# Kernel optimization log

Measured on AMD Instinct MI355X. Metric: run time of the kernel, lower is better.

Reference implementation:

```python
import jax, jax.numpy as jnp
import numpy as np

B, IN_DIM, HID, SUB_IN, SUB_OUT, GRID = 4096, 256, 512, 256, 256, 32
LN_EPS = 1e-5


def setup_inputs() -> dict:
    key = jax.random.key(0)
    ks = jax.random.split(key, 16)
    inp = {
        'x':  jax.random.normal(ks[0], (B, IN_DIM), jnp.float32),
        'h0': jax.random.normal(ks[1], (B, HID), jnp.float32),
        'c0': jax.random.normal(ks[2], (B, HID), jnp.float32),
        's0': jax.random.normal(ks[3], (B, SUB_OUT), jnp.float32),
        # LSTM gate params
        'kernel':  jax.random.normal(ks[4], (IN_DIM, 3 * HID), jnp.float32) * 0.05,
        'rkernel': jax.random.normal(ks[5], (HID, 3 * HID), jnp.float32) * 0.05,
        'bias':    jnp.zeros((3 * HID,), jnp.float32),
        # sub-layer recurrent mixing kernels (num_sub_layers=1)
        'sub_kx': jax.random.normal(ks[6], (1, IN_DIM, SUB_IN), jnp.float32) * 0.05,
        'sub_kh': jax.random.normal(ks[7], (1, SUB_OUT, SUB_IN), jnp.float32) * 0.05,
        'sub_tkan_kernel': jax.random.normal(ks[8], (1, 2 * SUB_OUT), jnp.float32) * 0.05,
        # Fourier KAN coefficients: (2, outdim, indim, gridsize) + bias
        'fc': jax.random.normal(ks[9], (2, SUB_OUT, SUB_IN, GRID), jnp.float32) / np.sqrt(SUB_IN * GRID),
        'fb': jnp.zeros((SUB_OUT,), jnp.float32),
        # aggregation + layer norm
        'agg_w': jax.random.normal(ks[10], (SUB_OUT, HID), jnp.float32) * 0.05,
        'agg_b': jnp.zeros((HID,), jnp.float32),
        'ln_g':  jnp.ones((HID,), jnp.float32),
        'ln_b':  jnp.zeros((HID,), jnp.float32),
    }
    return inp


def _fourier_kan(z, fc, fb):
    # z: [B, SUB_IN] -> [B, SUB_OUT]
    k = jnp.arange(1, GRID + 1, dtype=z.dtype)          # [G]
    ang = z[:, :, None] * k                             # [B, IN, G]
    return (jnp.einsum('big,oig->bo', jnp.cos(ang), fc[0])
            + jnp.einsum('big,oig->bo', jnp.sin(ang), fc[1]) + fb)


def reference(x, h0, c0, s0, kernel, rkernel, bias, sub_kx, sub_kh,
              sub_tkan_kernel, fc, fb, agg_w, agg_b, ln_g, ln_b):
    # LSTM-style gates (note: candidate also passes through sigmoid then tanh,
    # exactly as in the torch source)
    gates = jax.nn.sigmoid(x @ kernel + h0 @ rkernel + bias)      # [B, 3H]
    i, f, c_cand = jnp.split(gates, 3, axis=-1)
    c = f * c0 + i * jnp.tanh(c_cand)                             # [B, H]

    # single KAN sub-layer
    agg_in = x @ sub_kx[0] + s0 @ sub_kh[0]                       # [B, SUB_IN]
    sub_out = _fourier_kan(agg_in, fc, fb)                        # [B, SUB_OUT]
    rk_h, rk_x = jnp.split(sub_tkan_kernel[0], 2)                 # [SUB_OUT] each
    new_s = rk_h * sub_out + s0 * rk_x

    # aggregation -> output gate
    o = jax.nn.sigmoid(sub_out @ agg_w + agg_b)                   # [B, H]
    h = o * jnp.tanh(c)

    # layer norm
    mu = jnp.mean(h, axis=-1, keepdims=True)
    var = jnp.mean(jnp.square(h - mu), axis=-1, keepdims=True)
    h = (h - mu) * jax.lax.rsqrt(var + LN_EPS) * ln_g + ln_b
    return (h, c, new_s)
```

## Files before the change

### kernel.cpp

```cpp
#include <hip/hip_runtime.h>
#include <hip/hip_bf16.h>

typedef __bf16 bf16_t;
typedef __bf16 bf16x2 __attribute__((ext_vector_type(2)));
typedef __bf16 bf16x4 __attribute__((ext_vector_type(4)));
typedef __bf16 bf16x8 __attribute__((ext_vector_type(8)));
typedef float  f32x4  __attribute__((ext_vector_type(4)));

#define NB 4096
#define IN_DIM 256
#define HID 512
#define SUB 256
#define GRID_ 32

__device__ __forceinline__ float fract_f(float x) {
#if __has_builtin(__builtin_amdgcn_fractf)
  return __builtin_amdgcn_fractf(x);
#else
  return x - floorf(x);
#endif
}
__device__ __forceinline__ float cos_rev(float rev) {
#if __has_builtin(__builtin_amdgcn_cosf)
  return __builtin_amdgcn_cosf(rev);
#else
  return __cosf(rev * 6.283185307179586f);
#endif
}
__device__ __forceinline__ float sin_rev(float rev) {
#if __has_builtin(__builtin_amdgcn_sinf)
  return __builtin_amdgcn_sinf(rev);
#else
  return __sinf(rev * 6.283185307179586f);
#endif
}
__device__ __forceinline__ float sigm(float v) { return 1.f / (1.f + __expf(-v)); }
__device__ __forceinline__ float fast_tanh(float x) {
  float e = __expf(2.f * x);
  return (e - 1.f) / (e + 1.f);
}
#define INV2PI 0.15915494309189535f

#define O_XHI   0ull
#define O_XLO   2097152ull
#define O_H0    4194304ull
#define O_S0H   8388608ull
#define O_S0L   10485760ull
#define O_FCB   12582912ull
#define O_O     12582912ull
#define O_KT    20971520ull
#define O_RKT   21757952ull
#define O_AWT   23330816ull
#define O_KXH   23592960ull
#define O_KXL   23724032ull
#define O_KHH   23855104ull
#define O_KHL   23986176ull
#define O_TC    24117248ull
#define O_SOB   32505856ull
#define O_AGG   34603008ull
#define O_P3    38797312ull

__device__ __forceinline__ void tconv_body(const float* __restrict__ src,
                                           bf16_t* __restrict__ hi,
                                           bf16_t* __restrict__ lo,
                                           int R, int C, int bx, int by,
                                           bool wantlo, float scale) {
  __shared__ float t[32][33];
  int c0 = bx * 32, r0 = by * 32;
  int tx = threadIdx.x & 31, ty = threadIdx.x >> 5;
#pragma unroll
  for (int rr = 0; rr < 4; rr++) {
    int r = ty + rr * 8;
    t[r][tx] = src[(size_t)(r0 + r) * C + c0 + tx];
  }
  __syncthreads();
#pragma unroll
  for (int rr = 0; rr < 4; rr++) {
    int cl = ty + rr * 8;
    float f = t[tx][cl] * scale;
    bf16_t h = (bf16_t)f;
    size_t oi = (size_t)(c0 + cl) * R + r0 + tx;
    hi[oi] = h;
    if (wantlo) lo[oi] = (bf16_t)(f - (float)h);
  }
}

__global__ __launch_bounds__(256) void k_prep(const float* __restrict__ x,
                                              const float* __restrict__ h0,
                                              const float* __restrict__ s0,
                                              const float* __restrict__ fc,
                                              const float* __restrict__ Wk,
                                              const float* __restrict__ Wr,
                                              const float* __restrict__ aw,
                                              const float* __restrict__ kx,
                                              const float* __restrict__ kh,
                                              bf16_t* __restrict__ xhi, bf16_t* __restrict__ xlo,
                                              bf16_t* __restrict__ h0b,
                                              bf16_t* __restrict__ s0h, bf16_t* __restrict__ s0l,
                                              bf16_t* __restrict__ fcb2,
                                              bf16_t* __restrict__ kt,
                                              bf16_t* __restrict__ rkt,
                                              bf16_t* __restrict__ awt,
                                              bf16_t* __restrict__ kxh, bf16_t* __restrict__ kxl,
                                              bf16_t* __restrict__ khh, bf16_t* __restrict__ khl) {
  int bid = blockIdx.x;
  if (bid < 1024) {
    for (int q = bid * 256 + threadIdx.x; q < 1048576; q += 262144) {
      const float* src; bf16_t* hi; bf16_t* lo = nullptr; int base;
      if (q < 262144)       { src = x;  hi = xhi; lo = xlo; base = q; }
      else if (q < 786432)  { src = h0; hi = h0b;           base = q - 262144; }
      else                  { src = s0; hi = s0h; lo = s0l; base = q - 786432; }
      float4 v = *(const float4*)(src + (size_t)base * 4);
      bf16x4 h; h[0] = (bf16_t)v.x; h[1] = (bf16_t)v.y; h[2] = (bf16_t)v.z; h[3] = (bf16_t)v.w;
      *(bf16x4*)(hi + (size_t)base * 4) = h;
      if (lo) {
        bf16x4 l;
        l[0] = (bf16_t)(v.x - (float)h[0]); l[1] = (bf16_t)(v.y - (float)h[1]);
        l[2] = (bf16_t)(v.z - (float)h[2]); l[3] = (bf16_t)(v.w - (float)h[3]);
        *(bf16x4*)(lo + (size_t)base * 4) = l;
      }
    }
  } else if (bid < 3072) {
    __shared__ float tf[64 * 36];
    int tt = bid - 1024;
    int s = tt & 1, ot = (tt >> 1) & 3, i = tt >> 3;
    int o0 = ot * 64, nbb = ot >> 1, wnn = ot & 1;
    int row = threadIdx.x >> 2, col = (threadIdx.x & 3) * 8;
    const float* src = fc + ((size_t)s << 21) + ((size_t)(o0 + row) << 13) +
                       ((size_t)i << 5) + col;
    float4 v0 = *(const float4*)(src);
    float4 v1 = *(const float4*)(src + 4);
    *(float4*)(tf + row * 36 + col) = v0;
    *(float4*)(tf + row * 36 + col + 4) = v1;
    __syncthreads();
    int lr = threadIdx.x & 15, g4 = (threadIdx.x >> 4) & 3, j = threadIdx.x >> 6;
    const float* rp = tf + (j * 16 + lr) * 36 + g4 * 8;
    float4 a = *(const float4*)(rp);
    float4 b = *(const float4*)(rp + 4);
    bf16x8 h;
    h[0] = (bf16_t)a.x; h[1] = (bf16_t)a.y; h[2] = (bf16_t)a.z; h[3] = (bf16_t)a.w;
    h[4] = (bf16_t)b.x; h[5] = (bf16_t)b.y; h[6] = (bf16_t)b.z; h[7] = (bf16_t)b.w;
    size_t idx = (size_t)i * 16384 + nbb * 8192 + wnn * 4096 + j * 1024 +
                 s * 512 + g4 * 128 + lr * 8;
    *(bf16x8*)(fcb2 + idx) = h;
  } else {
    int b = bid - 3072;
    if (b < 384)       { tconv_body(Wk, kt,  nullptr, 256, 1536, b % 48, b / 48, false, 1.f); }
    else if (b < 1152) { b -= 384;  tconv_body(Wr, rkt, nullptr, 512, 1536, b % 48, b / 48, false, 1.f); }
    else if (b < 1280) { b -= 1152; tconv_body(aw, awt, nullptr, 256, 512,  b % 16, b / 16, false, 1.f); }
    else if (b < 1344) { b -= 1280; tconv_body(kx, kxh, kxl,     256, 256,  b % 8,  b / 8,  true, INV2PI); }
    else               { b -= 1344; tconv_body(kh, khh, khl,     256, 256,  b % 8,  b / 8,  true, INV2PI); }
  }
}

struct Pass { const bf16_t* A; const bf16_t* Bt; int K; int lda; int ldbt; };
struct GArgs {
  Pass p[6]; int np;
  const float* bias;
  int act;
  float* out; bf16_t* outb; int ldout;
};

template<int BM, int BN>
__global__ __launch_bounds__(512) void k_gemm(GArgs g) {
  constexpr int MI = BM / 32;
  constexpr int NJ = BN / 64;
  constexpr int IA = (BM * 8) / 512;
  constexpr int IB = (BN * 8) / 512;
  __shared__ bf16_t smA[BM * 64];
  __shared__ bf16_t smB[BN * 64];
  const int tid = threadIdx.x;
  const int m0 = blockIdx.y * BM, n0 = blockIdx.x * BN;
  const int wv = tid >> 6, lane = tid & 63;
  const int wm = wv >> 2, wn = wv & 3;
  const int lr = lane & 15, g4 = lane >> 4;

  f32x4 acc[MI][NJ];
#pragma unroll
  for (int i = 0; i < MI; i++)
#pragma unroll
    for (int j = 0; j < NJ; j++) acc[i][j] = f32x4{0.f, 0.f, 0.f, 0.f};

  for (int ps = 0; ps < g.np; ps++) {
    const bf16_t* A = g.p[ps].A;
    const bf16_t* Bt = g.p[ps].Bt;
    const int K = g.p[ps].K, lda = g.p[ps].lda, ldbt = g.p[ps].ldbt;
    for (int k0 = 0; k0 < K; k0 += 64) {
      bf16x8 ar[IA], br[IB];
#pragma unroll
      for (int r = 0; r < IA; r++) {
        int task = tid + r * 512, row = task >> 3, t = task & 7, sf = t ^ (row & 7);
        ar[r] = *(const bf16x8*)(A + (size_t)(m0 + row) * lda + k0 + sf * 8);
      }
#pragma unroll
      for (int r = 0; r < IB; r++) {
        int task = tid + r * 512, row = task >> 3, t = task & 7, sf = t ^ (row & 7);
        br[r] = *(const bf16x8*)(Bt + (size_t)(n0 + row) * ldbt + k0 + sf * 8);
      }
      __syncthreads();
#pragma unroll
      for (int r = 0; r < IA; r++) {
        int task = tid + r * 512, row = task >> 3, t = task & 7;
        *(bf16x8*)(smA + row * 64 + t * 8) = ar[r];
      }
#pragma unroll
      for (int r = 0; r < IB; r++) {
        int task = tid + r * 512, row = task >> 3, t = task & 7;
        *(bf16x8*)(smB + row * 64 + t * 8) = br[r];
      }
      __syncthreads();
#pragma unroll
      for (int ks = 0; ks < 2; ks++) {
        bf16x8 af[MI], bfr[NJ];
#pragma unroll
        for (int i = 0; i < MI; i++) {
          int row = wm * (BM / 2) + i * 16 + lr;
          af[i] = *(const bf16x8*)(smA + row * 64 + ((ks * 4 + g4) ^ (lr & 7)) * 8);
        }
#pragma unroll
        for (int j = 0; j < NJ; j++) {
          int row = wn * (BN / 4) + j * 16 + lr;
          bfr[j] = *(const bf16x8*)(smB + row * 64 + ((ks * 4 + g4) ^ (lr & 7)) * 8);
        }
#pragma unroll
        for (int i = 0; i < MI; i++)
#pragma unroll
          for (int j = 0; j < NJ; j++)
            acc[i][j] = __builtin_amdgcn_mfma_f32_16x16x32_bf16(af[i], bfr[j], acc[i][j], 0, 0, 0);
      }
    }
  }
#pragma unroll
  for (int i = 0; i < MI; i++)
#pragma unroll
    for (int j = 0; j < NJ; j++) {
      int col = n0 + wn * (BN / 4) + j * 16 + lr;
      float bb = g.bias ? g.bias[col] : 0.f;
#pragma unroll
      for (int r = 0; r < 4; r++) {
        int row = m0 + wm * (BM / 2) + i * 16 + (lane >> 4) * 4 + r;
        float v = acc[i][j][r] + bb;
        if (g.act == 1) v = sigm(v);
        if (g.outb) g.outb[(size_t)row * g.ldout + col] = (bf16_t)v;
        else        g.out [(size_t)row * g.ldout + col] = v;
      }
    }
}

struct GAArgs {
  const bf16_t* xhi; const bf16_t* h0b; const bf16_t* kt; const bf16_t* rkt;
  const float* bias; const float* c0; float* c_out; bf16_t* tc;
  const bf16_t* aggA[6]; const bf16_t* aggB[6];
  float* agg;
};

__global__ __launch_bounds__(256, 2) void k_gatesagg(GAArgs ga) {
  __shared__ bf16_t smA[64 * 64];
  __shared__ bf16_t smB[3 * 64 * 64];
  const int tid = threadIdx.x;
  const int wv = tid >> 6, lane = tid & 63;
  const int wm = wv >> 1, wn = wv & 1;
  const int lr = lane & 15, g4 = lane >> 4;

  if (blockIdx.x < 512) {
    const int b = blockIdx.x;
    const int n0 = (b & 7) * 64, m0 = (b >> 3) * 64;
    f32x4 acc[3][2][2];
#pragma unroll
    for (int t = 0; t < 3; t++)
#pragma unroll
      for (int i = 0; i < 2; i++)
#pragma unroll
        for (int j = 0; j < 2; j++) acc[t][i][j] = f32x4{0.f, 0.f, 0.f, 0.f};

    for (int ps = 0; ps < 2; ps++) {
      const bf16_t* A  = ps ? ga.h0b : ga.xhi;
      const bf16_t* Bt = ps ? ga.rkt : ga.kt;
      const int K = ps ? 512 : 256, ld = K;
      for (int k0 = 0; k0 < K; k0 += 64) {
        bf16x8 ar[2], br[6];
#pragma unroll
        for (int r = 0; r < 2; r++) {
          int task = tid + r * 256, row = task >> 3, t = task & 7, sf = t ^ (row & 7);
          ar[r] = *(const bf16x8*)(A + (size_t)(m0 + row) * ld + k0 + sf * 8);
        }
#pragma unroll
        for (int r = 0; r < 6; r++) {
          int task = tid + r * 256;
          int gate = task >> 9, rem = task & 511, o = rem >> 3, t = rem & 7, sf = t ^ (o & 7);
          br[r] = *(const bf16x8*)(Bt + (size_t)(gate * 512 + n0 + o) * ld + k0 + sf * 8);
        }
        __syncthreads();
#pragma unroll
        for (int r = 0; r < 2; r++) {
          int task = tid + r * 256, row = task >> 3, t = task & 7;
          *(bf16x8*)(smA + row * 64 + t * 8) = ar[r];
        }
#pragma unroll
        for (int r = 0; r < 6; r++) {
          int task = tid + r * 256;
          int gate = task >> 9, rem = task & 511, o = rem >> 3, t = rem & 7;
          *(bf16x8*)(smB + (gate * 64 + o) * 64 + t * 8) = br[r];
        }
        __syncthreads();
#pragma unroll
        for (int ks = 0; ks < 2; ks++) {
          bf16x8 af[2];
#pragma unroll
          for (int i = 0; i < 2; i++) {
            int row = wm * 32 + i * 16 + lr;
            af[i] = *(const bf16x8*)(smA + row * 64 + ((ks * 4 + g4) ^ (lr & 7)) * 8);
          }
#pragma unroll
          for (int t = 0; t < 3; t++) {
            bf16x8 bfr[2];
#pragma unroll
            for (int j = 0; j < 2; j++) {
              int row = wn * 32 + j * 16 + lr;
              bfr[j] = *(const bf16x8*)(smB + (t * 64 + row) * 64 + ((ks * 4 + g4) ^ (lr & 7)) * 8);
            }
#pragma unroll
            for (int i = 0; i < 2; i++)
#pragma unroll
              for (int j = 0; j < 2; j++)
                acc[t][i][j] = __builtin_amdgcn_mfma_f32_16x16x32_bf16(af[i], bfr[j], acc[t][i][j], 0, 0, 0);
          }
        }
      }
    }
#pragma unroll
    for (int i = 0; i < 2; i++)
#pragma unroll
      for (int j = 0; j < 2; j++) {
        int col = n0 + wn * 32 + j * 16 + lr;
        float bi = ga.bias[col], bf_ = ga.bias[512 + col], bc = ga.bias[1024 + col];
#pragma unroll
        for (int r = 0; r < 4; r++) {
          int row = m0 + wm * 32 + i * 16 + g4 * 4 + r;
          size_t idx = (size_t)row * 512 + col;
          float iv = sigm(acc[0][i][j][r] + bi);
          float fv = sigm(acc[1][i][j][r] + bf_);
          float cc = sigm(acc[2][i][j][r] + bc);
          float cv = fv * ga.c0[idx] + iv * fast_tanh(cc);
          ga.c_out[idx] = cv;
          ga.tc[idx] = (bf16_t)fast_tanh(cv);
        }
      }
  } else {
    const int b = blockIdx.x - 512;
    const int n0 = (b & 3) * 64, m0 = (b >> 2) * 64;
    f32x4 acc[2][2];
#pragma unroll
    for (int i = 0; i < 2; i++)
#pragma unroll
      for (int j = 0; j < 2; j++) acc[i][j] = f32x4{0.f, 0.f, 0.f, 0.f};

    for (int ps = 0; ps < 6; ps++) {
      const bf16_t* A  = ga.aggA[ps];
      const bf16_t* Bt = ga.aggB[ps];
      for (int k0 = 0; k0 < 256; k0 += 64) {
        bf16x8 ar[2], br[2];
#pragma unroll
        for (int r = 0; r < 2; r++) {
          int task = tid + r * 256, row = task >> 3, t = task & 7, sf = t ^ (row & 7);
          ar[r] = *(const bf16x8*)(A  + (size_t)(m0 + row) * 256 + k0 + sf * 8);
          br[r] = *(const bf16x8*)(Bt + (size_t)(n0 + row) * 256 + k0 + sf * 8);
        }
        __syncthreads();
#pragma unroll
        for (int r = 0; r < 2; r++) {
          int task = tid + r * 256, row = task >> 3, t = task & 7;
          *(bf16x8*)(smA + row * 64 + t * 8) = ar[r];
          *(bf16x8*)(smB + row * 64 + t * 8) = br[r];
        }
        __syncthreads();
#pragma unroll
        for (int ks = 0; ks < 2; ks++) {
          bf16x8 af[2], bfr[2];
#pragma unroll
          for (int i = 0; i < 2; i++) {
            int row = wm * 32 + i * 16 + lr;
            af[i] = *(const bf16x8*)(smA + row * 64 + ((ks * 4 + g4) ^ (lr & 7)) * 8);
          }
#pragma unroll
          for (int j = 0; j < 2; j++) {
            int row = wn * 32 + j * 16 + lr;
            bfr[j] = *(const bf16x8*)(smB + row * 64 + ((ks * 4 + g4) ^ (lr & 7)) * 8);
          }
#pragma unroll
          for (int i = 0; i < 2; i++)
#pragma unroll
            for (int j = 0; j < 2; j++)
              acc[i][j] = __builtin_amdgcn_mfma_f32_16x16x32_bf16(af[i], bfr[j], acc[i][j], 0, 0, 0);
        }
      }
    }
#pragma unroll
    for (int i = 0; i < 2; i++)
#pragma unroll
      for (int j = 0; j < 2; j++) {
        int col = n0 + wn * 32 + j * 16 + lr;
#pragma unroll
        for (int r = 0; r < 4; r++) {
          int row = m0 + wm * 32 + i * 16 + g4 * 4 + r;
          ga.agg[(size_t)row * 256 + col] = acc[i][j][r];
        }
      }
  }
}

struct FArgs { const float* agg; const bf16_t* fcb2; bf16_t* P[8]; };

__global__ __launch_bounds__(128, 2) void k_fourier(FArgs fa) {
  __shared__ float  zl[64 * 33];
  __shared__ bf16_t Asm[2][64 * 64];
  const int tid = threadIdx.x;
  const int bx = blockIdx.x;
  const int q = bx & 7, nb = (bx >> 3) & 1, mb = bx >> 4;
  const int m0 = mb * 64, n0 = nb * 128, i0 = q * 32;
  const int wv = tid >> 6, lane = tid & 63;
  const int wn = wv;
  const int lr = lane & 15, g4 = lane >> 4;

#pragma unroll
  for (int r = 0; r < 4; r++) {
    int task = tid + r * 128, row = task >> 3, seg = task & 7;
    float4 v = *(const float4*)(fa.agg + (size_t)(m0 + row) * 256 + i0 + seg * 4);
    zl[row * 33 + seg * 4 + 0] = v.x;
    zl[row * 33 + seg * 4 + 1] = v.y;
    zl[row * 33 + seg * 4 + 2] = v.z;
    zl[row * 33 + seg * 4 + 3] = v.w;
  }

  const bf16_t* pB = fa.fcb2 + (size_t)i0 * 16384 + nb * 8192 + wn * 4096 + lane * 8;
  auto loadB = [&](int i, bf16x8 (&b)[8]) {
#pragma unroll
    for (int ks = 0; ks < 2; ks++)
#pragma unroll
      for (int j = 0; j < 4; j++)
        b[ks * 4 + j] = *(const bf16x8*)(pB + (size_t)i * 16384 + j * 1024 + ks * 512);
  };

  const int grow = tid >> 1, hp = tid & 1;
  const float* zp = zl + grow * 33;
  const int as0 = grow * 64 + (((2 * hp    ) ^ (grow & 7)) * 8);
  const int as1 = grow * 64 + (((2 * hp + 1) ^ (grow & 7)) * 8);
  const int as2 = grow * 64 + (((4 + 2 * hp) ^ (grow & 7)) * 8);
  const int as3 = grow * 64 + (((5 + 2 * hp) ^ (grow & 7)) * 8);
  auto genA = [&](int i, bf16_t* Ab) {
    float zr = zp[i];
    bf16x8 c0v, c1v, s0v, s1v;
#pragma unroll
    for (int t = 0; t < 8; t++) {
      float r0 = fract_f(zr * (float)(hp * 16 + t + 1));
      float r1 = fract_f(zr * (float)(hp * 16 + 8 + t + 1));
      c0v[t] = (bf16_t)cos_rev(r0); s0v[t] = (bf16_t)sin_rev(r0);
      c1v[t] = (bf16_t)cos_rev(r1); s1v[t] = (bf16_t)sin_rev(r1);
    }
    *(bf16x8*)(Ab + as0) = c0v;
    *(bf16x8*)(Ab + as1) = c1v;
    *(bf16x8*)(Ab + as2) = s0v;
    *(bf16x8*)(Ab + as3) = s1v;
  };

  int offA[8];
#pragma unroll
  for (int ks = 0; ks < 2; ks++)
#pragma unroll
    for (int i4 = 0; i4 < 4; i4++)
      offA[ks * 4 + i4] = (i4 * 16 + lr) * 64 + ((ks * 4 + g4) ^ (lr & 7)) * 8;

  f32x4 acc[4][4];
#pragma unroll
  for (int i = 0; i < 4; i++)
#pragma unroll
    for (int j = 0; j < 4; j++) acc[i][j] = f32x4{0.f, 0.f, 0.f, 0.f};

  auto domfma = [&](const bf16x8 (&af)[8], const bf16x8 (&b)[8]) {
    __builtin_amdgcn_s_setprio(1);
#pragma unroll
    for (int ks = 0; ks < 2; ks++)
#pragma unroll
      for (int i4 = 0; i4 < 4; i4++)
#pragma unroll
        for (int j = 0; j < 4; j++)
          acc[i4][j] = __builtin_amdgcn_mfma_f32_16x16x32_bf16(af[ks * 4 + i4], b[ks * 4 + j], acc[i4][j], 0, 0, 0);
    __builtin_amdgcn_s_setprio(0);
  };
  auto readA = [&](const bf16_t* Ac, bf16x8 (&af)[8]) {
#pragma unroll
    for (int t = 0; t < 8; t++) af[t] = *(const bf16x8*)(Ac + offA[t]);
  };

  bf16x8 bA_[8], bB_[8];
  __syncthreads();
  loadB(0, bA_);
  genA(0, Asm[0]);
  asm volatile("s_waitcnt lgkmcnt(0)" ::: "memory");
  __builtin_amdgcn_s_barrier();

#pragma unroll 1
  for (int it = 0; it < 16; it++) {
    const int i = it * 2;
    bf16x8 af[8];
    if (i < 31) loadB(i + 1, bB_);
    readA(Asm[0], af);
    if (i < 31) genA(i + 1, Asm[1]);
    domfma(af, bA_);
    asm volatile("s_waitcnt lgkmcnt(0)" ::: "memory");
    __builtin_amdgcn_s_barrier();
    if (i + 2 < 32) loadB(i + 2, bA_);
    readA(Asm[1], af);
    if (i + 2 < 32) genA(i + 2, Asm[0]);
    domfma(af, bB_);
    asm volatile("s_waitcnt lgkmcnt(0)" ::: "memory");
    __builtin_amdgcn_s_barrier();
  }

  bf16_t* outp = fa.P[q];
#pragma unroll
  for (int i = 0; i < 4; i++)
#pragma unroll
    for (int j = 0; j < 4; j++) {
      int col = n0 + wn * 64 + j * 16 + lr;
#pragma unroll
      for (int r = 0; r < 4; r++) {
        int row = m0 + i * 16 + g4 * 4 + r;
        outp[(size_t)row * 256 + col] = (bf16_t)acc[i][j][r];
      }
    }
}

struct RArgs {
  const bf16_t* P[8];
  const float* fb; const float* tk; const float* s0;
  float* news; bf16_t* sob;
};

__global__ __launch_bounds__(256) void k_freduce(RArgs ra) {
  int stride = gridDim.x * blockDim.x;
  for (int qd = blockIdx.x * blockDim.x + threadIdx.x; qd < 262144; qd += stride) {
    int i = qd * 4, o = i & 255;
    float4 v = {0.f, 0.f, 0.f, 0.f};
#pragma unroll
    for (int c = 0; c < 8; c++) {
      bf16x4 p = *(const bf16x4*)(ra.P[c] + i);
      v.x += (float)p[0]; v.y += (float)p[1]; v.z += (float)p[2]; v.w += (float)p[3];
    }
    v.x += ra.fb[o + 0]; v.y += ra.fb[o + 1]; v.z += ra.fb[o + 2]; v.w += ra.fb[o + 3];
    bf16x4 sb; sb[0] = (bf16_t)v.x; sb[1] = (bf16_t)v.y; sb[2] = (bf16_t)v.z; sb[3] = (bf16_t)v.w;
    *(bf16x4*)(ra.sob + i) = sb;
    float4 s = *(const float4*)(ra.s0 + i);
    float4 ns;
    ns.x = ra.tk[o + 0] * v.x + ra.tk[256 + o + 0] * s.x;
    ns.y = ra.tk[o + 1] * v.y + ra.tk[256 + o + 1] * s.y;
    ns.z = ra.tk[o + 2] * v.z + ra.tk[256 + o + 2] * s.z;
    ns.w = ra.tk[o + 3] * v.w + ra.tk[256 + o + 3] * s.w;
    *(float4*)(ra.news + i) = ns;
  }
}

__global__ __launch_bounds__(256) void k_ln(const bf16_t* __restrict__ o,
                                            const bf16_t* __restrict__ tc,
                                            const float* __restrict__ lg,
                                            const float* __restrict__ lb,
                                            float* __restrict__ h) {
  int b = blockIdx.x, tid = threadIdx.x;
  bf16x2 ov = *(const bf16x2*)(o + (size_t)b * 512 + tid * 2);
  bf16x2 tv = *(const bf16x2*)(tc + (size_t)b * 512 + tid * 2);
  float h0 = (float)ov[0] * (float)tv[0], h1 = (float)ov[1] * (float)tv[1];
  float s = h0 + h1, ss = h0 * h0 + h1 * h1;
#pragma unroll
  for (int off = 32; off; off >>= 1) {
    s += __shfl_xor(s, off);
    ss += __shfl_xor(ss, off);
  }
  __shared__ float red[8];
  int wid = tid >> 6;
  if ((tid & 63) == 0) { red[wid] = s; red[4 + wid] = ss; }
  __syncthreads();
  s = red[0] + red[1] + red[2] + red[3];
  ss = red[4] + red[5] + red[6] + red[7];
  float mu = s * (1.f / 512.f);
  float var = ss * (1.f / 512.f) - mu * mu;
  float rs = rsqrtf(var + 1e-5f);
  int j = tid * 2;
  h[(size_t)b * 512 + j]     = (h0 - mu) * rs * lg[j]     + lb[j];
  h[(size_t)b * 512 + j + 1] = (h1 - mu) * rs * lg[j + 1] + lb[j + 1];
}

extern "C" void kernel_launch(void* const* d_in, const int* in_sizes, int n_in,
                              void* d_out, int out_size, void* d_ws, size_t ws_size,
                              hipStream_t stream) {
  const float* x    = (const float*)d_in[0];
  const float* h0   = (const float*)d_in[1];
  const float* c0   = (const float*)d_in[2];
  const float* s0   = (const float*)d_in[3];
  const float* Wk   = (const float*)d_in[4];
  const float* Wr   = (const float*)d_in[5];
  const float* bias = (const float*)d_in[6];
  const float* kx   = (const float*)d_in[7];
  const float* kh   = (const float*)d_in[8];
  const float* tk   = (const float*)d_in[9];
  const float* fc   = (const float*)d_in[10];
  const float* fb   = (const float*)d_in[11];
  const float* aw   = (const float*)d_in[12];
  const float* ab   = (const float*)d_in[13];
  const float* lg   = (const float*)d_in[14];
  const float* lbp  = (const float*)d_in[15];
  float* out = (float*)d_out;
  char* ws = (char*)d_ws;
  auto BF = [&](unsigned long long off) { return (bf16_t*)(ws + off); };
  auto FP = [&](unsigned long long off) { return (float*)(ws + off); };

  k_prep<<<4480, 256, 0, stream>>>(x, h0, s0, fc, Wk, Wr, aw, kx, kh,
                                   BF(O_XHI), BF(O_XLO), BF(O_H0),
                                   BF(O_S0H), BF(O_S0L), BF(O_FCB),
                                   BF(O_KT), BF(O_RKT), BF(O_AWT),
                                   BF(O_KXH), BF(O_KXL), BF(O_KHH), BF(O_KHL));

  {
    GAArgs ga{};
    ga.xhi = BF(O_XHI); ga.h0b = BF(O_H0); ga.kt = BF(O_KT); ga.rkt = BF(O_RKT);
    ga.bias = bias; ga.c0 = c0; ga.c_out = out + 2097152; ga.tc = BF(O_TC);
    ga.aggA[0] = BF(O_XHI); ga.aggB[0] = BF(O_KXH);
    ga.aggA[1] = BF(O_XHI); ga.aggB[1] = BF(O_KXL);
    ga.aggA[2] = BF(O_XLO); ga.aggB[2] = BF(O_KXH);
    ga.aggA[3] = BF(O_S0H); ga.aggB[3] = BF(O_KHH);
    ga.aggA[4] = BF(O_S0H); ga.aggB[4] = BF(O_KHL);
    ga.aggA[5] = BF(O_S0L); ga.aggB[5] = BF(O_KHH);
    ga.agg = FP(O_AGG);
    k_gatesagg<<<768, 256, 0, stream>>>(ga);
  }

  FArgs fa;
  fa.agg = FP(O_AGG); fa.fcb2 = BF(O_FCB);
  for (int c = 0; c < 6; c++) fa.P[c] = BF((unsigned long long)c * 2097152ull);
  fa.P[6] = BF(O_P3);
  fa.P[7] = BF(O_P3 + 2097152ull);
  k_fourier<<<1024, 128, 0, stream>>>(fa);

  RArgs ra;
  for (int c = 0; c < 8; c++) ra.P[c] = fa.P[c];
  ra.fb = fb; ra.tk = tk; ra.s0 = s0;
  ra.news = out + 4194304; ra.sob = BF(O_SOB);
  k_freduce<<<1024, 256, 0, stream>>>(ra);

  {
    GArgs g{};
    g.p[0] = { BF(O_SOB), BF(O_AWT), 256, 256, 256 };
    g.np = 1; g.bias = ab; g.act = 1;
    g.out = nullptr; g.outb = BF(O_O); g.ldout = 512;
    k_gemm<64, 128><<<dim3(4, 64), 512, 0, stream>>>(g);
  }
  k_ln<<<4096, 256, 0, stream>>>(BF(O_O), BF(O_TC), lg, lbp, out);
}
```

Baseline: 95.88 us.

## Fuse Fourier partial reduction and new_s update into output-projection GEMM

Removes the separate reduction kernel. The sigmoid output-projection GEMM now sums the eight bf16 partial Fourier buffers while loading its A tile, adds the bias, and the first column-block also writes new_s. This eliminates one kernel launch and the intermediate bf16 sub_out buffer round-trip. In exchange, each of the four N-blocks re-reads all partial buffers, quadrupling the partial-sum reads, which must be served from cache to pay off.

```diff
diff --git a/kernel.cpp b/kernel.cpp
--- a/kernel.cpp
+++ b/kernel.cpp
@@ -56,7 +56,6 @@
 #define O_KHH   23855104ull
 #define O_KHL   23986176ull
 #define O_TC    24117248ull
-#define O_SOB   32505856ull
 #define O_AGG   34603008ull
 #define O_P3    38797312ull
 
@@ -153,100 +152,6 @@
   }
 }
 
-struct Pass { const bf16_t* A; const bf16_t* Bt; int K; int lda; int ldbt; };
-struct GArgs {
-  Pass p[6]; int np;
-  const float* bias;
-  int act;
-  float* out; bf16_t* outb; int ldout;
-};
-
-template<int BM, int BN>
-__global__ __launch_bounds__(512) void k_gemm(GArgs g) {
-  constexpr int MI = BM / 32;
-  constexpr int NJ = BN / 64;
-  constexpr int IA = (BM * 8) / 512;
-  constexpr int IB = (BN * 8) / 512;
-  __shared__ bf16_t smA[BM * 64];
-  __shared__ bf16_t smB[BN * 64];
-  const int tid = threadIdx.x;
-  const int m0 = blockIdx.y * BM, n0 = blockIdx.x * BN;
-  const int wv = tid >> 6, lane = tid & 63;
-  const int wm = wv >> 2, wn = wv & 3;
-  const int lr = lane & 15, g4 = lane >> 4;
-
-  f32x4 acc[MI][NJ];
-#pragma unroll
-  for (int i = 0; i < MI; i++)
-#pragma unroll
-    for (int j = 0; j < NJ; j++) acc[i][j] = f32x4{0.f, 0.f, 0.f, 0.f};
-
-  for (int ps = 0; ps < g.np; ps++) {
-    const bf16_t* A = g.p[ps].A;
-    const bf16_t* Bt = g.p[ps].Bt;
-    const int K = g.p[ps].K, lda = g.p[ps].lda, ldbt = g.p[ps].ldbt;
-    for (int k0 = 0; k0 < K; k0 += 64) {
-      bf16x8 ar[IA], br[IB];
-#pragma unroll
-      for (int r = 0; r < IA; r++) {
-        int task = tid + r * 512, row = task >> 3, t = task & 7, sf = t ^ (row & 7);
-        ar[r] = *(const bf16x8*)(A + (size_t)(m0 + row) * lda + k0 + sf * 8);
-      }
-#pragma unroll
-      for (int r = 0; r < IB; r++) {
-        int task = tid + r * 512, row = task >> 3, t = task & 7, sf = t ^ (row & 7);
-        br[r] = *(const bf16x8*)(Bt + (size_t)(n0 + row) * ldbt + k0 + sf * 8);
-      }
-      __syncthreads();
-#pragma unroll
-      for (int r = 0; r < IA; r++) {
-        int task = tid + r * 512, row = task >> 3, t = task & 7;
-        *(bf16x8*)(smA + row * 64 + t * 8) = ar[r];
-      }
-#pragma unroll
-      for (int r = 0; r < IB; r++) {
-        int task = tid + r * 512, row = task >> 3, t = task & 7;
-        *(bf16x8*)(smB + row * 64 + t * 8) = br[r];
-      }
-      __syncthreads();
-#pragma unroll
-      for (int ks = 0; ks < 2; ks++) {
-        bf16x8 af[MI], bfr[NJ];
-#pragma unroll
-        for (int i = 0; i < MI; i++) {
-          int row = wm * (BM / 2) + i * 16 + lr;
-          af[i] = *(const bf16x8*)(smA + row * 64 + ((ks * 4 + g4) ^ (lr & 7)) * 8);
-        }
-#pragma unroll
-        for (int j = 0; j < NJ; j++) {
-          int row = wn * (BN / 4) + j * 16 + lr;
-          bfr[j] = *(const bf16x8*)(smB + row * 64 + ((ks * 4 + g4) ^ (lr & 7)) * 8);
-        }
-#pragma unroll
-        for (int i = 0; i < MI; i++)
-#pragma unroll
-          for (int j = 0; j < NJ; j++)
-            acc[i][j] = __builtin_amdgcn_mfma_f32_16x16x32_bf16(af[i], bfr[j], acc[i][j], 0, 0, 0);
-      }
-    }
-  }
-#pragma unroll
-  for (int i = 0; i < MI; i++)
-#pragma unroll
-    for (int j = 0; j < NJ; j++) {
-      int col = n0 + wn * (BN / 4) + j * 16 + lr;
-      float bb = g.bias ? g.bias[col] : 0.f;
-#pragma unroll
-      for (int r = 0; r < 4; r++) {
-        int row = m0 + wm * (BM / 2) + i * 16 + (lane >> 4) * 4 + r;
-        float v = acc[i][j][r] + bb;
-        if (g.act == 1) v = sigm(v);
-        if (g.outb) g.outb[(size_t)row * g.ldout + col] = (bf16_t)v;
-        else        g.out [(size_t)row * g.ldout + col] = v;
-      }
-    }
-}
-
 struct GAArgs {
   const bf16_t* xhi; const bf16_t* h0b; const bf16_t* kt; const bf16_t* rkt;
   const float* bias; const float* c0; float* c_out; bf16_t* tc;
@@ -531,33 +436,107 @@
     }
 }
 
-struct RArgs {
+struct OPArgs {
   const bf16_t* P[8];
   const float* fb; const float* tk; const float* s0;
-  float* news; bf16_t* sob;
+  const bf16_t* awt; const float* ab;
+  float* news; bf16_t* o;
 };
 
-__global__ __launch_bounds__(256) void k_freduce(RArgs ra) {
-  int stride = gridDim.x * blockDim.x;
-  for (int qd = blockIdx.x * blockDim.x + threadIdx.x; qd < 262144; qd += stride) {
-    int i = qd * 4, o = i & 255;
-    float4 v = {0.f, 0.f, 0.f, 0.f};
+__global__ __launch_bounds__(512) void k_oproj(OPArgs a) {
+  __shared__ bf16_t smA[64 * 64];
+  __shared__ bf16_t smB[128 * 64];
+  const int tid = threadIdx.x;
+  const int n0 = blockIdx.x * 128;
+  const int m0 = blockIdx.y * 64;
+  const int wv = tid >> 6, lane = tid & 63;
+  const int wm = wv >> 2, wn = wv & 3;
+  const int lr = lane & 15, g4 = lane >> 4;
+
+  f32x4 acc[2][2];
+#pragma unroll
+  for (int i = 0; i < 2; i++)
+#pragma unroll
+    for (int j = 0; j < 2; j++) acc[i][j] = f32x4{0.f, 0.f, 0.f, 0.f};
+
+  for (int k0 = 0; k0 < 256; k0 += 64) {
+    const int arow = tid >> 3, at = tid & 7, asf = at ^ (arow & 7);
+    const int acol = k0 + asf * 8;
+    const size_t aoff = (size_t)(m0 + arow) * 256 + acol;
+    float av[8] = {0.f, 0.f, 0.f, 0.f, 0.f, 0.f, 0.f, 0.f};
 #pragma unroll
     for (int c = 0; c < 8; c++) {
-      bf16x4 p = *(const bf16x4*)(ra.P[c] + i);
-      v.x += (float)p[0]; v.y += (float)p[1]; v.z += (float)p[2]; v.w += (float)p[3];
-    }
-    v.x += ra.fb[o + 0]; v.y += ra.fb[o + 1]; v.z += ra.fb[o + 2]; v.w += ra.fb[o + 3];
-    bf16x4 sb; sb[0] = (bf16_t)v.x; sb[1] = (bf16_t)v.y; sb[2] = (bf16_t)v.z; sb[3] = (bf16_t)v.w;
-    *(bf16x4*)(ra.sob + i) = sb;
-    float4 s = *(const float4*)(ra.s0 + i);
-    float4 ns;
-    ns.x = ra.tk[o + 0] * v.x + ra.tk[256 + o + 0] * s.x;
-    ns.y = ra.tk[o + 1] * v.y + ra.tk[256 + o + 1] * s.y;
-    ns.z = ra.tk[o + 2] * v.z + ra.tk[256 + o + 2] * s.z;
-    ns.w = ra.tk[o + 3] * v.w + ra.tk[256 + o + 3] * s.w;
-    *(float4*)(ra.news + i) = ns;
-  }
+      bf16x8 p = *(const bf16x8*)(a.P[c] + aoff);
+#pragma unroll
+      for (int t2 = 0; t2 < 8; t2++) av[t2] += (float)p[t2];
+    }
+#pragma unroll
+    for (int t2 = 0; t2 < 8; t2++) av[t2] += a.fb[acol + t2];
+    if (blockIdx.x == 0) {
+      float4 sa = *(const float4*)(a.s0 + aoff);
+      float4 sb = *(const float4*)(a.s0 + aoff + 4);
+      float sv[8] = {sa.x, sa.y, sa.z, sa.w, sb.x, sb.y, sb.z, sb.w};
+      float4 n0v, n1v;
+      n0v.x = a.tk[acol + 0] * av[0] + a.tk[256 + acol + 0] * sv[0];
+      n0v.y = a.tk[acol + 1] * av[1] + a.tk[256 + acol + 1] * sv[1];
+      n0v.z = a.tk[acol + 2] * av[2] + a.tk[256 + acol + 2] * sv[2];
+      n0v.w = a.tk[acol + 3] * av[3] + a.tk[256 + acol + 3] * sv[3];
+      n1v.x = a.tk[acol + 4] * av[4] + a.tk[256 + acol + 4] * sv[4];
+      n1v.y = a.tk[acol + 5] * av[5] + a.tk[256 + acol + 5] * sv[5];
+      n1v.z = a.tk[acol + 6] * av[6] + a.tk[256 + acol + 6] * sv[6];
+      n1v.w = a.tk[acol + 7] * av[7] + a.tk[256 + acol + 7] * sv[7];
+      *(float4*)(a.news + aoff) = n0v;
+      *(float4*)(a.news + aoff + 4) = n1v;
+    }
+    bf16x8 ah;
+#pragma unroll
+    for (int t2 = 0; t2 < 8; t2++) ah[t2] = (bf16_t)av[t2];
+    bf16x8 br[2];
+#pragma unroll
+    for (int r = 0; r < 2; r++) {
+      int task = tid + r * 512, row = task >> 3, t = task & 7, sf = t ^ (row & 7);
+      br[r] = *(const bf16x8*)(a.awt + (size_t)(n0 + row) * 256 + k0 + sf * 8);
+    }
+    __syncthreads();
+    *(bf16x8*)(smA + arow * 64 + at * 8) = ah;
+#pragma unroll
+    for (int r = 0; r < 2; r++) {
+      int task = tid + r * 512, row = task >> 3, t = task & 7;
+      *(bf16x8*)(smB + row * 64 + t * 8) = br[r];
+    }
+    __syncthreads();
+#pragma unroll
+    for (int ks = 0; ks < 2; ks++) {
+      bf16x8 af[2], bfr[2];
+#pragma unroll
+      for (int i = 0; i < 2; i++) {
+        int row = wm * 32 + i * 16 + lr;
+        af[i] = *(const bf16x8*)(smA + row * 64 + ((ks * 4 + g4) ^ (lr & 7)) * 8);
+      }
+#pragma unroll
+      for (int j = 0; j < 2; j++) {
+        int row = wn * 32 + j * 16 + lr;
+        bfr[j] = *(const bf16x8*)(smB + row * 64 + ((ks * 4 + g4) ^ (lr & 7)) * 8);
+      }
+#pragma unroll
+      for (int i = 0; i < 2; i++)
+#pragma unroll
+        for (int j = 0; j < 2; j++)
+          acc[i][j] = __builtin_amdgcn_mfma_f32_16x16x32_bf16(af[i], bfr[j], acc[i][j], 0, 0, 0);
+    }
+  }
+#pragma unroll
+  for (int i = 0; i < 2; i++)
+#pragma unroll
+    for (int j = 0; j < 2; j++) {
+      int col = n0 + wn * 32 + j * 16 + lr;
+      float bb = a.ab[col];
+#pragma unroll
+      for (int r = 0; r < 4; r++) {
+        int row = m0 + wm * 32 + i * 16 + g4 * 4 + r;
+        a.o[(size_t)row * 512 + col] = (bf16_t)sigm(acc[i][j][r] + bb);
+      }
+    }
 }
 
 __global__ __launch_bounds__(256) void k_ln(const bf16_t* __restrict__ o,
@@ -640,18 +619,13 @@
   fa.P[7] = BF(O_P3 + 2097152ull);
   k_fourier<<<1024, 128, 0, stream>>>(fa);
 
-  RArgs ra;
-  for (int c = 0; c < 8; c++) ra.P[c] = fa.P[c];
-  ra.fb = fb; ra.tk = tk; ra.s0 = s0;
-  ra.news = out + 4194304; ra.sob = BF(O_SOB);
-  k_freduce<<<1024, 256, 0, stream>>>(ra);
-
   {
-    GArgs g{};
-    g.p[0] = { BF(O_SOB), BF(O_AWT), 256, 256, 256 };
-    g.np = 1; g.bias = ab; g.act = 1;
-    g.out = nullptr; g.outb = BF(O_O); g.ldout = 512;
-    k_gemm<64, 128><<<dim3(4, 64), 512, 0, stream>>>(g);
+    OPArgs oa{};
+    for (int c = 0; c < 8; c++) oa.P[c] = fa.P[c];
+    oa.fb = fb; oa.tk = tk; oa.s0 = s0;
+    oa.awt = BF(O_AWT); oa.ab = ab;
+    oa.news = out + 4194304; oa.o = BF(O_O);
+    k_oproj<<<dim3(4, 64), 512, 0, stream>>>(oa);
   }
   k_ln<<<4096, 256, 0, stream>>>(BF(O_O), BF(O_TC), lg, lbp, out);
 }
```

New measurement: 99.91 us. 4.2% more time.
